# Kernel optimization log

Measured on AMD Instinct MI355X. Metric: run time of the kernel, lower is better.

Reference implementation:

```python
import jax, jax.numpy as jnp
import numpy as np

B, N, F_IN, F_OUT, H = 8, 1024, 128, 64, 4
EPS = 1e-7
NEG_SLOPE = 0.2


def setup_inputs() -> dict:
    key = jax.random.key(0)
    k_a, k_x, k_w, k_aw, k_ab = jax.random.split(key, 5)
    A = jax.random.randint(k_a, (B, N, N), 0, 2).astype(jnp.float32)
    x = jax.random.normal(k_x, (B, N, F_IN), dtype=jnp.float32)
    # per-head params (stacked over head axis): GAT.W (xavier-normal-ish), attention Linear(2F->1)
    W = jax.random.normal(k_w, (H, F_IN, F_OUT), dtype=jnp.float32) * np.sqrt(2.0 / (F_IN + F_OUT))
    lim = 1.0 / np.sqrt(2 * F_OUT)
    a_w = jax.random.uniform(k_aw, (H, 2 * F_OUT), minval=-lim, maxval=lim, dtype=jnp.float32)
    a_b = jax.random.uniform(k_ab, (H,), minval=-lim, maxval=lim, dtype=jnp.float32)
    return {"A": A, "x": x, "W": W, "a_w": a_w, "a_b": a_b}


def reference(A, x, W, a_w, a_b):
    # Wh: (B, H, N, F_OUT)
    Wh = jnp.einsum('bnf,hfo->bhno', x, W)
    # attention linear on concat([Wh_i, Wh_j]) is separable: a1.Wh_i + a2.Wh_j + b
    a1, a2 = a_w[:, :F_OUT], a_w[:, F_OUT:]
    s_i = jnp.einsum('bhno,ho->bhn', Wh, a1)   # depends on row index i (dim 1 of (B,N,N))
    s_j = jnp.einsum('bhno,ho->bhn', Wh, a2)   # depends on col index j (dim 2)
    e = s_i[:, :, :, None] + s_j[:, :, None, :] + a_b[None, :, None, None]  # (B,H,Ni,Nj)
    e = jnp.where(e >= 0, e, NEG_SLOPE * e)  # LeakyReLU(0.2)
    # masked softmax as in source: exp, mask by A, normalize over dim=1 of (B,N,N) -> axis 2 here
    exps = jnp.exp(e) * A[:, None, :, :]
    attn = exps / (jnp.sum(exps, axis=2, keepdims=True) + EPS)
    out = jnp.einsum('bhij,bhjo->bhio', attn, Wh)  # matmul over j
    # concat heads on feature dim: (B, N, H*F_OUT)
    return out.transpose(0, 2, 1, 3).reshape(B, N, H * F_OUT)
```

## Files before the change

### kernel.cpp

```cpp
#include <hip/hip_runtime.h>
#include <hip/hip_bf16.h>
#include <hip/hip_fp16.h>

#define BB 8
#define NN 1024
#define FIN 128
#define FOUT 64
#define HH 4
#define EPSV 1e-7f
#define SLOPE 0.2f
#define LOG2E 1.44269504088896340736f

typedef _Float16 v8h __attribute__((ext_vector_type(8)));
typedef _Float16 v4h __attribute__((ext_vector_type(4)));
typedef float v4f __attribute__((ext_vector_type(4)));

__global__ __launch_bounds__(256) void k0_wt(const float* __restrict__ W,
                                             _Float16* __restrict__ Wtt) {
  for (int it = 0; it < 16; ++it) {
    int idx = blockIdx.x * 4096 + it * 256 + threadIdx.x;
    int e = idx & 7, ln = (idx >> 3) & 15, kgg = (idx >> 7) & 15,
        ct = idx >> 11;
    int c = ct * 16 + ln, k = kgg * 8 + e;
    Wtt[idx] = (_Float16)W[(size_t)(c >> 6) * 8192 + k * 64 + (c & 63)];
  }
}

__global__ __launch_bounds__(256) void k1_whm(const float* __restrict__ x,
                                              const _Float16* __restrict__ Wtt,
                                              const float* __restrict__ aw,
                                              const float* __restrict__ ab,
                                              _Float16* __restrict__ WhH,
                                              float* __restrict__ si2,
                                              float* __restrict__ tj2) {
  __shared__ _Float16 xs[16][136];
  int tid = threadIdx.x;
#pragma unroll
  for (int t2 = 0; t2 < 2; ++t2) {
    int idx = t2 * 256 + tid;
    int row = idx >> 5, c4 = (idx & 31) * 4;
    float4 v = *(const float4*)(x + ((size_t)blockIdx.x * 16 + row) * FIN + c4);
    v4h hv;
    hv[0] = (_Float16)v.x; hv[1] = (_Float16)v.y;
    hv[2] = (_Float16)v.z; hv[3] = (_Float16)v.w;
    *(v4h*)(&xs[row][c4]) = hv;
  }
  __syncthreads();
  int w = tid >> 6, l = tid & 63;
  int kg = l >> 4, ln = l & 15;
  v4f acc[4] = {{}, {}, {}, {}};
#pragma unroll
  for (int ks = 0; ks < 4; ++ks) {
    v8h af = *(const v8h*)(&xs[ln][ks * 32 + kg * 8]);
    int kgg = ks * 4 + kg;
#pragma unroll
    for (int t = 0; t < 4; ++t) {
      int ct = w * 4 + t;
      v8h bf = *(const v8h*)(Wtt + (((size_t)ct * 16 + kgg) * 16 + ln) * 8);
      acc[t] = __builtin_amdgcn_mfma_f32_16x16x32_f16(af, bf, acc[t], 0, 0, 0);
    }
  }
  float a1v[4], a2v[4];
#pragma unroll
  for (int t = 0; t < 4; ++t) {
    a1v[t] = aw[w * 128 + t * 16 + ln];
    a2v[t] = aw[w * 128 + 64 + t * 16 + ln];
  }
  float abv = ab[w];
#pragma unroll
  for (int r = 0; r < 4; ++r) {
    float v1 = acc[0][r] * a1v[0] + acc[1][r] * a1v[1] +
               acc[2][r] * a1v[2] + acc[3][r] * a1v[3];
    float v2 = acc[0][r] * a2v[0] + acc[1][r] * a2v[1] +
               acc[2][r] * a2v[2] + acc[3][r] * a2v[3];
#pragma unroll
    for (int off = 1; off < 16; off <<= 1) {
      v1 += __shfl_xor(v1, off);
      v2 += __shfl_xor(v2, off);
    }
    if (ln == 0) {
      int gr = blockIdx.x * 16 + kg * 4 + r;
      int b_ = gr >> 10, n_ = gr & 1023;
      size_t row = ((size_t)b_ * HH + w) * NN + n_;
      si2[row] = v1 * LOG2E;
      tj2[row] = (v2 + abv) * LOG2E;
    }
  }
#pragma unroll
  for (int t = 0; t < 4; ++t) {
#pragma unroll
    for (int r = 0; r < 4; ++r) {
      int gr = blockIdx.x * 16 + kg * 4 + r;
      int b_ = gr >> 10, n_ = gr & 1023;
      WhH[(((size_t)b_ * HH + w) * NN + n_) * 64 + (t * 16 + ln)] =
          (_Float16)acc[t][r];
    }
  }
}

__global__ __launch_bounds__(256) void k2_colsum(const float* __restrict__ A,
                                                 const float* __restrict__ si2,
                                                 const float* __restrict__ tj2,
                                                 float* __restrict__ part) {
  __shared__ float sil[4][32];
  int b = blockIdx.z, is = blockIdx.y, jt = blockIdx.x;
  int tid = threadIdx.x;
  int j = jt * 256 + tid;
  int i0 = is * 32;
  if (tid < 128) {
    int h = tid >> 5, ii = tid & 31;
    sil[h][ii] = si2[((size_t)(b * HH + h)) * NN + i0 + ii];
  }
  __syncthreads();
  float tjv[4], acc[4] = {0.f, 0.f, 0.f, 0.f};
#pragma unroll
  for (int h = 0; h < 4; ++h) tjv[h] = tj2[((size_t)(b * HH + h)) * NN + j];
  const float* Ap = A + ((size_t)b * NN + i0) * NN + j;
#pragma unroll 4
  for (int ii = 0; ii < 32; ++ii) {
    float a = Ap[(size_t)ii * NN];
#pragma unroll
    for (int h = 0; h < 4; ++h) {
      float f = sil[h][ii] + tjv[h];
      float g = fmaxf(f, SLOPE * f);
      acc[h] += a * __builtin_amdgcn_exp2f(g);
    }
  }
#pragma unroll
  for (int h = 0; h < 4; ++h)
    part[((size_t)(is * 32) + b * HH + h) * NN + j] = acc[h];
}

__global__ __launch_bounds__(256) void k3_scale_tr(
    const _Float16* __restrict__ WhH, const float* __restrict__ part,
    _Float16* __restrict__ VTt) {
  __shared__ float rbuf[64];
  __shared__ _Float16 tile[64 * 66];
  int bid = blockIdx.x;
  int b = bid & 7, rest = bid >> 3;
  int h = rest & 3, jt = rest >> 2;
  int bh = b * HH + h, j0 = jt * 64;
  int tid = threadIdx.x;
  if (tid < 64) {
    float s = 0.f;
#pragma unroll
    for (int is = 0; is < 32; ++is)
      s += part[((size_t)(is * 32) + bh) * NN + j0 + tid];
    rbuf[tid] = 1.0f / (s + EPSV);
  }
  __syncthreads();
#pragma unroll
  for (int it = 0; it < 16; ++it) {
    int lin = it * 256 + tid;
    int jj = lin >> 6, o = lin & 63;
    float v = (float)WhH[((size_t)bh * NN + j0 + jj) * 64 + o] * rbuf[jj];
    tile[o * 66 + jj] = (_Float16)v;
  }
  __syncthreads();
#pragma unroll
  for (int it = 0; it < 16; ++it) {
    int lin = it * 256 + tid;
    int o = lin >> 6, jj64 = lin & 63;
    int j = j0 + jj64;
    int jb = j >> 5, jj = j & 31;
    VTt[(((size_t)bh * 32 + jb) * 64 + o) * 32 + jj] = tile[o * 66 + jj64];
  }
}

__global__ __launch_bounds__(256) void k4_pv(const float* __restrict__ A,
                                             const float* __restrict__ si2,
                                             const float* __restrict__ tj2,
                                             const _Float16* __restrict__ VTt,
                                             float* __restrict__ out) {
  __shared__ _Float16 Ah[32][1032];
  __shared__ float tjl[4][1024];
  __shared__ float sil[4][32];
  int bid = blockIdx.x;
  int b = bid & 7, it = bid >> 3;
  int i0 = it * 32;
  int tid = threadIdx.x;
#pragma unroll
  for (int t2 = 0; t2 < 16; ++t2) {
    int idx = t2 * 256 + tid;
    int h = idx >> 10, j = idx & 1023;
    tjl[h][j] = tj2[((size_t)(b * HH + h)) * NN + j];
  }
  if (tid < 128) {
    int h = tid >> 5, ii = tid & 31;
    sil[h][ii] = si2[((size_t)(b * HH + h)) * NN + i0 + ii];
  }
  const float* Ab = A + ((size_t)b * NN + i0) * NN;
#pragma unroll 8
  for (int t2 = 0; t2 < 32; ++t2) {
    int idx = t2 * 256 + tid;
    int row = idx >> 8, c = (idx & 255) * 4;
    float4 v = *(const float4*)(Ab + (size_t)row * NN + c);
    v4h hv;
    hv[0] = (_Float16)v.x; hv[1] = (_Float16)v.y;
    hv[2] = (_Float16)v.z; hv[3] = (_Float16)v.w;
    *(v4h*)(&Ah[row][c]) = hv;
  }
  __syncthreads();

  int w = tid >> 6, l = tid & 63;
  int kg = l >> 4, ln = l & 15;
  float si0 = sil[w][ln];
  float si1 = sil[w][16 + ln];
  int bh = b * HH + w;
  v4f acc0[4] = {{}, {}, {}, {}};
  v4f acc1[4] = {{}, {}, {}, {}};
  const _Float16* VTb = VTt + (size_t)bh * 32 * 64 * 32;
  const float* tj = tjl[w];

#define PEXP(si, av, tv) \
  ((float)(av) * \
   __builtin_amdgcn_exp2f(fmaxf((si) + (tv), SLOPE * ((si) + (tv)))))

#pragma unroll 2
  for (int jb = 0; jb < 32; ++jb) {
    int j = jb * 32 + kg * 8;
    v8h ar0 = *(const v8h*)(&Ah[ln][j]);
    v8h ar1 = *(const v8h*)(&Ah[16 + ln][j]);
    float4 t0 = *(const float4*)(tj + j);
    float4 t1 = *(const float4*)(tj + j + 4);
    v8h af0, af1;
    af0[0] = (_Float16)PEXP(si0, ar0[0], t0.x);
    af0[1] = (_Float16)PEXP(si0, ar0[1], t0.y);
    af0[2] = (_Float16)PEXP(si0, ar0[2], t0.z);
    af0[3] = (_Float16)PEXP(si0, ar0[3], t0.w);
    af0[4] = (_Float16)PEXP(si0, ar0[4], t1.x);
    af0[5] = (_Float16)PEXP(si0, ar0[5], t1.y);
    af0[6] = (_Float16)PEXP(si0, ar0[6], t1.z);
    af0[7] = (_Float16)PEXP(si0, ar0[7], t1.w);
    af1[0] = (_Float16)PEXP(si1, ar1[0], t0.x);
    af1[1] = (_Float16)PEXP(si1, ar1[1], t0.y);
    af1[2] = (_Float16)PEXP(si1, ar1[2], t0.z);
    af1[3] = (_Float16)PEXP(si1, ar1[3], t0.w);
    af1[4] = (_Float16)PEXP(si1, ar1[4], t1.x);
    af1[5] = (_Float16)PEXP(si1, ar1[5], t1.y);
    af1[6] = (_Float16)PEXP(si1, ar1[6], t1.z);
    af1[7] = (_Float16)PEXP(si1, ar1[7], t1.w);
    const _Float16* vb = VTb + (size_t)jb * 2048 + kg * 8;
    v8h b0 = *(const v8h*)(vb + (0 * 16 + ln) * 32);
    v8h b1 = *(const v8h*)(vb + (1 * 16 + ln) * 32);
    v8h b2 = *(const v8h*)(vb + (2 * 16 + ln) * 32);
    v8h b3 = *(const v8h*)(vb + (3 * 16 + ln) * 32);
    acc0[0] = __builtin_amdgcn_mfma_f32_16x16x32_f16(af0, b0, acc0[0], 0, 0, 0);
    acc1[0] = __builtin_amdgcn_mfma_f32_16x16x32_f16(af1, b0, acc1[0], 0, 0, 0);
    acc0[1] = __builtin_amdgcn_mfma_f32_16x16x32_f16(af0, b1, acc0[1], 0, 0, 0);
    acc1[1] = __builtin_amdgcn_mfma_f32_16x16x32_f16(af1, b1, acc1[1], 0, 0, 0);
    acc0[2] = __builtin_amdgcn_mfma_f32_16x16x32_f16(af0, b2, acc0[2], 0, 0, 0);
    acc1[2] = __builtin_amdgcn_mfma_f32_16x16x32_f16(af1, b2, acc1[2], 0, 0, 0);
    acc0[3] = __builtin_amdgcn_mfma_f32_16x16x32_f16(af0, b3, acc0[3], 0, 0, 0);
    acc1[3] = __builtin_amdgcn_mfma_f32_16x16x32_f16(af1, b3, acc1[3], 0, 0, 0);
  }
#undef PEXP

#pragma unroll
  for (int r = 0; r < 4; ++r) {
    int gi0 = i0 + kg * 4 + r;
    float* op0 = out + ((size_t)b * NN + gi0) * 256 + w * 64;
    op0[0 * 16 + ln] = acc0[0][r];
    op0[1 * 16 + ln] = acc0[1][r];
    op0[2 * 16 + ln] = acc0[2][r];
    op0[3 * 16 + ln] = acc0[3][r];
    float* op1 = op0 + 16 * 256;
    op1[0 * 16 + ln] = acc1[0][r];
    op1[1 * 16 + ln] = acc1[1][r];
    op1[2 * 16 + ln] = acc1[2][r];
    op1[3 * 16 + ln] = acc1[3][r];
  }
}

extern "C" void kernel_launch(void* const* d_in, const int* in_sizes, int n_in,
                              void* d_out, int out_size, void* d_ws,
                              size_t ws_size, hipStream_t stream) {
  const float* A = (const float*)d_in[0];
  const float* x = (const float*)d_in[1];
  const float* W = (const float*)d_in[2];
  const float* aw = (const float*)d_in[3];
  const float* ab = (const float*)d_in[4];
  float* out = (float*)d_out;
  char* ws = (char*)d_ws;
  _Float16* WhH = (_Float16*)ws;
  _Float16* VTt = (_Float16*)(ws + (4u << 20));
  _Float16* Wtt = (_Float16*)(ws + (8u << 20));
  float* si2 = (float*)(ws + (8u << 20) + (256u << 10));
  float* tj2 = (float*)(ws + (8u << 20) + (384u << 10));
  float* part = (float*)(ws + (8u << 20) + (512u << 10));

  hipLaunchKernelGGL(k0_wt, dim3(8), dim3(256), 0, stream, W, Wtt);
  hipLaunchKernelGGL(k1_whm, dim3(512), dim3(256), 0, stream, x, Wtt, aw, ab,
                     WhH, si2, tj2);
  hipLaunchKernelGGL(k2_colsum, dim3(4, 32, BB), dim3(256), 0, stream, A, si2,
                     tj2, part);
  hipLaunchKernelGGL(k3_scale_tr, dim3(512), dim3(256), 0, stream, WhH, part,
                     VTt);
  hipLaunchKernelGGL(k4_pv, dim3(256), dim3(256), 0, stream, A, si2, tj2, VTt,
                     out);
}
```

Baseline: 48.05 us.

## Pack adjacency mask into bits during colsum and split PV over j halves

The column-sum kernel now processes 64 rows per block and writes a ballot-packed bitmask of A alongside the partial sums. The PV kernel reads this compact bitmask instead of re-reading the full fp32 adjacency matrix, which cuts its global traffic and LDS footprint. PV now uses 512 threads, with two waves per head each covering half of j, and reduces their partial accumulators through shared memory. The risks are the extra bitmask stores in the colsum kernel, the added reduction and synchronisation, and the assumption that A holds only 0/1 values.

Result: slower. 62.26 us (+29.6%).

```diff
diff --git a/kernel.cpp b/kernel.cpp
--- a/kernel.cpp
+++ b/kernel.cpp
@@ -98,17 +98,18 @@
   }
 }
 
-__global__ __launch_bounds__(256) void k2_colsum(const float* __restrict__ A,
-                                                 const float* __restrict__ si2,
-                                                 const float* __restrict__ tj2,
-                                                 float* __restrict__ part) {
-  __shared__ float sil[4][32];
+__global__ __launch_bounds__(256) void kb_colsum_bits(
+    const float* __restrict__ A, const float* __restrict__ si2,
+    const float* __restrict__ tj2, float* __restrict__ part,
+    unsigned long long* __restrict__ Abits) {
+  __shared__ float sil[4][64];
   int b = blockIdx.z, is = blockIdx.y, jt = blockIdx.x;
   int tid = threadIdx.x;
+  int w = tid >> 6;
   int j = jt * 256 + tid;
-  int i0 = is * 32;
-  if (tid < 128) {
-    int h = tid >> 5, ii = tid & 31;
+  int i0 = is * 64;
+  if (tid < 256) {
+    int h = tid >> 6, ii = tid & 63;
     sil[h][ii] = si2[((size_t)(b * HH + h)) * NN + i0 + ii];
   }
   __syncthreads();
@@ -117,8 +118,11 @@
   for (int h = 0; h < 4; ++h) tjv[h] = tj2[((size_t)(b * HH + h)) * NN + j];
   const float* Ap = A + ((size_t)b * NN + i0) * NN + j;
 #pragma unroll 4
-  for (int ii = 0; ii < 32; ++ii) {
+  for (int ii = 0; ii < 64; ++ii) {
     float a = Ap[(size_t)ii * NN];
+    unsigned long long m = __ballot(a != 0.0f);
+    if ((tid & 63) == 0)
+      Abits[((size_t)b * NN + i0 + ii) * 16 + jt * 4 + w] = m;
 #pragma unroll
     for (int h = 0; h < 4; ++h) {
       float f = sil[h][ii] + tjv[h];
@@ -144,7 +148,7 @@
   if (tid < 64) {
     float s = 0.f;
 #pragma unroll
-    for (int is = 0; is < 32; ++is)
+    for (int is = 0; is < 16; ++is)
       s += part[((size_t)(is * 32) + bh) * NN + j0 + tid];
     rbuf[tid] = 1.0f / (s + EPSV);
   }
@@ -167,21 +171,21 @@
   }
 }
 
-__global__ __launch_bounds__(256) void k4_pv(const float* __restrict__ A,
-                                             const float* __restrict__ si2,
-                                             const float* __restrict__ tj2,
-                                             const _Float16* __restrict__ VTt,
-                                             float* __restrict__ out) {
-  __shared__ _Float16 Ah[32][1032];
+__global__ __launch_bounds__(512) void k4_pv(
+    const unsigned long long* __restrict__ Abits,
+    const float* __restrict__ si2, const float* __restrict__ tj2,
+    const _Float16* __restrict__ VTt, float* __restrict__ out) {
+  __shared__ unsigned long long Ab[32][17];
   __shared__ float tjl[4][1024];
   __shared__ float sil[4][32];
+  __shared__ float red[4][64][33];
   int bid = blockIdx.x;
   int b = bid & 7, it = bid >> 3;
   int i0 = it * 32;
   int tid = threadIdx.x;
 #pragma unroll
-  for (int t2 = 0; t2 < 16; ++t2) {
-    int idx = t2 * 256 + tid;
+  for (int t2 = 0; t2 < 8; ++t2) {
+    int idx = t2 * 512 + tid;
     int h = idx >> 10, j = idx & 1023;
     tjl[h][j] = tj2[((size_t)(b * HH + h)) * NN + j];
   }
@@ -189,58 +193,53 @@
     int h = tid >> 5, ii = tid & 31;
     sil[h][ii] = si2[((size_t)(b * HH + h)) * NN + i0 + ii];
   }
-  const float* Ab = A + ((size_t)b * NN + i0) * NN;
-#pragma unroll 8
-  for (int t2 = 0; t2 < 32; ++t2) {
-    int idx = t2 * 256 + tid;
-    int row = idx >> 8, c = (idx & 255) * 4;
-    float4 v = *(const float4*)(Ab + (size_t)row * NN + c);
-    v4h hv;
-    hv[0] = (_Float16)v.x; hv[1] = (_Float16)v.y;
-    hv[2] = (_Float16)v.z; hv[3] = (_Float16)v.w;
-    *(v4h*)(&Ah[row][c]) = hv;
+  {
+    int row = tid >> 4, word = tid & 15;
+    Ab[row][word] = Abits[((size_t)b * NN + i0 + row) * 16 + word];
   }
   __syncthreads();
 
   int w = tid >> 6, l = tid & 63;
+  int h = w & 3, jh = w >> 2;
   int kg = l >> 4, ln = l & 15;
-  float si0 = sil[w][ln];
-  float si1 = sil[w][16 + ln];
-  int bh = b * HH + w;
+  float si0 = sil[h][ln];
+  float si1 = sil[h][16 + ln];
+  int bh = b * HH + h;
   v4f acc0[4] = {{}, {}, {}, {}};
   v4f acc1[4] = {{}, {}, {}, {}};
   const _Float16* VTb = VTt + (size_t)bh * 32 * 64 * 32;
-  const float* tj = tjl[w];
-
-#define PEXP(si, av, tv) \
-  ((float)(av) * \
-   __builtin_amdgcn_exp2f(fmaxf((si) + (tv), SLOPE * ((si) + (tv)))))
+  const float* tj = tjl[h];
+  int jbase = jh * 512;
+
+#define PEXP(si, tv) \
+  __builtin_amdgcn_exp2f(fmaxf((si) + (tv), SLOPE * ((si) + (tv))))
 
 #pragma unroll 2
-  for (int jb = 0; jb < 32; ++jb) {
-    int j = jb * 32 + kg * 8;
-    v8h ar0 = *(const v8h*)(&Ah[ln][j]);
-    v8h ar1 = *(const v8h*)(&Ah[16 + ln][j]);
+  for (int jq = 0; jq < 16; ++jq) {
+    int j = jbase + jq * 32 + kg * 8;
+    int widx = j >> 6, sh = j & 63;
+    unsigned int bits0 = (unsigned int)(Ab[ln][widx] >> sh) & 0xffu;
+    unsigned int bits1 = (unsigned int)(Ab[16 + ln][widx] >> sh) & 0xffu;
     float4 t0 = *(const float4*)(tj + j);
     float4 t1 = *(const float4*)(tj + j + 4);
     v8h af0, af1;
-    af0[0] = (_Float16)PEXP(si0, ar0[0], t0.x);
-    af0[1] = (_Float16)PEXP(si0, ar0[1], t0.y);
-    af0[2] = (_Float16)PEXP(si0, ar0[2], t0.z);
-    af0[3] = (_Float16)PEXP(si0, ar0[3], t0.w);
-    af0[4] = (_Float16)PEXP(si0, ar0[4], t1.x);
-    af0[5] = (_Float16)PEXP(si0, ar0[5], t1.y);
-    af0[6] = (_Float16)PEXP(si0, ar0[6], t1.z);
-    af0[7] = (_Float16)PEXP(si0, ar0[7], t1.w);
-    af1[0] = (_Float16)PEXP(si1, ar1[0], t0.x);
-    af1[1] = (_Float16)PEXP(si1, ar1[1], t0.y);
-    af1[2] = (_Float16)PEXP(si1, ar1[2], t0.z);
-    af1[3] = (_Float16)PEXP(si1, ar1[3], t0.w);
-    af1[4] = (_Float16)PEXP(si1, ar1[4], t1.x);
-    af1[5] = (_Float16)PEXP(si1, ar1[5], t1.y);
-    af1[6] = (_Float16)PEXP(si1, ar1[6], t1.z);
-    af1[7] = (_Float16)PEXP(si1, ar1[7], t1.w);
-    const _Float16* vb = VTb + (size_t)jb * 2048 + kg * 8;
+    af0[0] = (bits0 & 1u) ? (_Float16)PEXP(si0, t0.x) : (_Float16)0;
+    af0[1] = (bits0 & 2u) ? (_Float16)PEXP(si0, t0.y) : (_Float16)0;
+    af0[2] = (bits0 & 4u) ? (_Float16)PEXP(si0, t0.z) : (_Float16)0;
+    af0[3] = (bits0 & 8u) ? (_Float16)PEXP(si0, t0.w) : (_Float16)0;
+    af0[4] = (bits0 & 16u) ? (_Float16)PEXP(si0, t1.x) : (_Float16)0;
+    af0[5] = (bits0 & 32u) ? (_Float16)PEXP(si0, t1.y) : (_Float16)0;
+    af0[6] = (bits0 & 64u) ? (_Float16)PEXP(si0, t1.z) : (_Float16)0;
+    af0[7] = (bits0 & 128u) ? (_Float16)PEXP(si0, t1.w) : (_Float16)0;
+    af1[0] = (bits1 & 1u) ? (_Float16)PEXP(si1, t0.x) : (_Float16)0;
+    af1[1] = (bits1 & 2u) ? (_Float16)PEXP(si1, t0.y) : (_Float16)0;
+    af1[2] = (bits1 & 4u) ? (_Float16)PEXP(si1, t0.z) : (_Float16)0;
+    af1[3] = (bits1 & 8u) ? (_Float16)PEXP(si1, t0.w) : (_Float16)0;
+    af1[4] = (bits1 & 16u) ? (_Float16)PEXP(si1, t1.x) : (_Float16)0;
+    af1[5] = (bits1 & 32u) ? (_Float16)PEXP(si1, t1.y) : (_Float16)0;
+    af1[6] = (bits1 & 64u) ? (_Float16)PEXP(si1, t1.z) : (_Float16)0;
+    af1[7] = (bits1 & 128u) ? (_Float16)PEXP(si1, t1.w) : (_Float16)0;
+    const _Float16* vb = VTb + (size_t)(j >> 5) * 2048 + kg * 8;
     v8h b0 = *(const v8h*)(vb + (0 * 16 + ln) * 32);
     v8h b1 = *(const v8h*)(vb + (1 * 16 + ln) * 32);
     v8h b2 = *(const v8h*)(vb + (2 * 16 + ln) * 32);
@@ -256,19 +255,38 @@
   }
 #undef PEXP
 
-#pragma unroll
-  for (int r = 0; r < 4; ++r) {
-    int gi0 = i0 + kg * 4 + r;
-    float* op0 = out + ((size_t)b * NN + gi0) * 256 + w * 64;
-    op0[0 * 16 + ln] = acc0[0][r];
-    op0[1 * 16 + ln] = acc0[1][r];
-    op0[2 * 16 + ln] = acc0[2][r];
-    op0[3 * 16 + ln] = acc0[3][r];
-    float* op1 = op0 + 16 * 256;
-    op1[0 * 16 + ln] = acc1[0][r];
-    op1[1 * 16 + ln] = acc1[1][r];
-    op1[2 * 16 + ln] = acc1[2][r];
-    op1[3 * 16 + ln] = acc1[3][r];
+  if (jh) {
+#pragma unroll
+    for (int t = 0; t < 4; ++t)
+#pragma unroll
+      for (int r = 0; r < 4; ++r) {
+        red[h][l][t * 4 + r] = acc0[t][r];
+        red[h][l][16 + t * 4 + r] = acc1[t][r];
+      }
+  }
+  __syncthreads();
+  if (!jh) {
+#pragma unroll
+    for (int t = 0; t < 4; ++t)
+#pragma unroll
+      for (int r = 0; r < 4; ++r) {
+        acc0[t][r] += red[h][l][t * 4 + r];
+        acc1[t][r] += red[h][l][16 + t * 4 + r];
+      }
+#pragma unroll
+    for (int r = 0; r < 4; ++r) {
+      int gi0 = i0 + kg * 4 + r;
+      float* op0 = out + ((size_t)b * NN + gi0) * 256 + h * 64;
+      op0[0 * 16 + ln] = acc0[0][r];
+      op0[1 * 16 + ln] = acc0[1][r];
+      op0[2 * 16 + ln] = acc0[2][r];
+      op0[3 * 16 + ln] = acc0[3][r];
+      float* op1 = op0 + 16 * 256;
+      op1[0 * 16 + ln] = acc1[0][r];
+      op1[1 * 16 + ln] = acc1[1][r];
+      op1[2 * 16 + ln] = acc1[2][r];
+      op1[3 * 16 + ln] = acc1[3][r];
+    }
   }
 }
 
@@ -288,14 +306,16 @@
   float* si2 = (float*)(ws + (8u << 20) + (256u << 10));
   float* tj2 = (float*)(ws + (8u << 20) + (384u << 10));
   float* part = (float*)(ws + (8u << 20) + (512u << 10));
+  unsigned long long* Abits =
+      (unsigned long long*)(ws + (10u << 20) + (512u << 10));
 
   hipLaunchKernelGGL(k0_wt, dim3(8), dim3(256), 0, stream, W, Wtt);
   hipLaunchKernelGGL(k1_whm, dim3(512), dim3(256), 0, stream, x, Wtt, aw, ab,
                      WhH, si2, tj2);
-  hipLaunchKernelGGL(k2_colsum, dim3(4, 32, BB), dim3(256), 0, stream, A, si2,
-                     tj2, part);
+  hipLaunchKernelGGL(kb_colsum_bits, dim3(4, 16, BB), dim3(256), 0, stream, A,
+                     si2, tj2, part, Abits);
   hipLaunchKernelGGL(k3_scale_tr, dim3(512), dim3(256), 0, stream, WhH, part,
                      VTt);
-  hipLaunchKernelGGL(k4_pv, dim3(256), dim3(256), 0, stream, A, si2, tj2, VTt,
-                     out);
-}
+  hipLaunchKernelGGL(k4_pv, dim3(256), dim3(512), 0, stream, Abits, si2, tj2,
+                     VTt, out);
+}
```
